# Optimization experiments

Hardware: AMD Instinct MI355X
Metric: run time of the kernel (lower is better)

## Reference

```python
import jax, jax.numpy as jnp
import numpy as np

B, T, P, D, S, R = 4, 128, 256, 512, 64, 8  # batch, window, patches, d_model, n_state, dt_rank


def setup_inputs() -> dict:
    key = jax.random.key(0)
    ks = jax.random.split(key, 8)
    sc = 0.02  # weight init scale
    return {
        "X": jax.random.normal(ks[0], (B, T, P, D), jnp.float32),
        "H0": jnp.zeros((B, P, S), jnp.float32),
        "a_hat": jax.random.normal(ks[1], (S,), jnp.float32),
        "U_w": jax.random.normal(ks[2], (S, D), jnp.float32) * sc,
        "sB_w": jax.random.normal(ks[3], (S, D), jnp.float32) * sc,
        "sB_b": jnp.zeros((S,), jnp.float32),
        "sC_w": jax.random.normal(ks[4], (S, D), jnp.float32) * sc,
        "sC_b": jnp.zeros((S,), jnp.float32),
        "sD1_w": jax.random.normal(ks[5], (R, D), jnp.float32) * sc,
        "sD1_b": jnp.zeros((R,), jnp.float32),
        "sD2_w": jax.random.normal(ks[6], (1, R), jnp.float32) * sc,
        "sD2_b": jnp.zeros((1,), jnp.float32),
        "ro_w": jax.random.normal(ks[7], (D, S), jnp.float32) * sc,
    }


def reference(X, H0, a_hat, U_w, sB_w, sB_b, sC_w, sC_b, sD1_w, sD1_b, sD2_w, sD2_b, ro_w):
    eps = 1e-12
    logA = -jnp.exp(a_hat)                                    # [S]
    # selective (input-dependent) parameters
    u = jnp.einsum('btpd,sd->btps', X, U_w)                   # [B,T,P,S]
    B_t = jnp.einsum('btpd,sd->btps', X, sB_w) + sB_b
    C_t = jnp.einsum('btpd,sd->btps', X, sC_w) + sC_b
    dt_feat = jax.nn.silu(jnp.einsum('btpd,rd->btpr', X, sD1_w) + sD1_b)
    dt = jax.nn.softplus(jnp.einsum('btpr,or->btpo', dt_feat, sD2_w) + sD2_b)  # [B,T,P,1]
    A = jnp.exp(dt * logA)                                    # [B,T,P,S] via broadcast
    b = (1.0 - A) * (B_t * u)
    # prefix-product scan: h_t = A_t*h_{t-1} + b_t  ->  h_t = P_t*(H0 + cumsum(b/P))
    Pc = jnp.cumprod(jnp.maximum(A, eps), axis=1)             # [B,T,P,S]
    invP = 1.0 / jnp.maximum(Pc, eps)
    c = jnp.cumsum(b * invP, axis=1)
    H_seq = Pc * (H0[:, None] + c)                            # [B,T,P,S]
    Y_seq = jnp.einsum('btps,ds->btpd', C_t * H_seq, ro_w)    # [B,T,P,D]
    Y_seq = Y_seq.reshape(X.shape[0], -1, X.shape[-1])        # [B, T*P, D]
    H_T = H_seq[:, -1]                                        # [B,P,S]
    return (H_seq, Y_seq, H_T)
```

## Files before the change

kernel.cpp:

```cpp
#include <hip/hip_runtime.h>
#include <math.h>

namespace {
constexpr int B_N = 4;
constexpr int T_N = 128;
constexpr int P_N = 256;
constexpr int D_N = 512;
constexpr int S_N = 64;
constexpr int NTH = 512;
constexpr int KC  = 64;

constexpr int XS_OFF  = 0;
constexpr int WS_OFF  = 16384;
constexpr int UB_OFF  = 0;
constexpr int BB_OFF  = 32768;
constexpr int CH_OFF  = 49152;
constexpr int ROS_OFF = 0;
constexpr int DT_OFF  = 65536;
constexpr int LA_OFF  = 66048;
constexpr int LDS_BYTES = 66304;
}

typedef short bf16x8 __attribute__((ext_vector_type(8)));
typedef float f32x4  __attribute__((ext_vector_type(4)));

__device__ __forceinline__ unsigned short f2b(float f) {
    unsigned int x = __float_as_uint(f);
    return (unsigned short)((x + 0x7FFFu + ((x >> 16) & 1u)) >> 16);
}
__device__ __forceinline__ float b2f(unsigned short h) {
    return __uint_as_float(((unsigned int)h) << 16);
}
__device__ __forceinline__ int swz(int row, int col) {
    return row * 64 + (col ^ ((row & 7) << 3));
}

__device__ __forceinline__ void stage16(unsigned short* tile, int row, int col0,
                                        const float* __restrict__ src) {
    float4 v0 = *(const float4*)(src);
    float4 v1 = *(const float4*)(src + 4);
    float4 v2 = *(const float4*)(src + 8);
    float4 v3 = *(const float4*)(src + 12);
    bf16x8 h0, h1;
    h0[0] = (short)f2b(v0.x); h0[1] = (short)f2b(v0.y); h0[2] = (short)f2b(v0.z); h0[3] = (short)f2b(v0.w);
    h0[4] = (short)f2b(v1.x); h0[5] = (short)f2b(v1.y); h0[6] = (short)f2b(v1.z); h0[7] = (short)f2b(v1.w);
    h1[0] = (short)f2b(v2.x); h1[1] = (short)f2b(v2.y); h1[2] = (short)f2b(v2.z); h1[3] = (short)f2b(v2.w);
    h1[4] = (short)f2b(v3.x); h1[5] = (short)f2b(v3.y); h1[6] = (short)f2b(v3.z); h1[7] = (short)f2b(v3.w);
    *(bf16x8*)&tile[swz(row, col0)]     = h0;
    *(bf16x8*)&tile[swz(row, col0 + 8)] = h1;
}

__global__ __launch_bounds__(NTH, 4) void mamba_mfma(
    const float* __restrict__ X, const float* __restrict__ H0,
    const float* __restrict__ a_hat,
    const float* __restrict__ U_w, const float* __restrict__ sB_w, const float* __restrict__ sB_b,
    const float* __restrict__ sC_w, const float* __restrict__ sC_b,
    const float* __restrict__ sD1_w, const float* __restrict__ sD1_b,
    const float* __restrict__ sD2_w, const float* __restrict__ sD2_b,
    const float* __restrict__ ro_w,
    float* __restrict__ Hseq, float* __restrict__ Y, float* __restrict__ HT)
{
    __shared__ __align__(16) char smem[LDS_BYTES];
    unsigned short* XS  = (unsigned short*)(smem + XS_OFF);
    unsigned short* WS  = (unsigned short*)(smem + WS_OFF);
    float*          UBUF= (float*)(smem + UB_OFF);
    unsigned short* BBUF= (unsigned short*)(smem + BB_OFF);
    unsigned short* ROS = (unsigned short*)(smem + ROS_OFF);
    unsigned short* CHB = (unsigned short*)(smem + CH_OFF);
    float*          DTB = (float*)(smem + DT_OFF);
    float*          LA  = (float*)(smem + LA_OFF);

    const int tid  = threadIdx.x;
    const int lane = tid & 63;
    const int wid  = tid >> 6;
    const int wm   = wid >> 2;
    const int wn   = wid & 3;
    const int l15  = lane & 15;
    const int lg   = lane >> 4;
    const int b    = blockIdx.x >> 8;
    const int p    = blockIdx.x & 255;

    if (tid < S_N) LA[tid] = -expf(a_hat[tid]);
    if (tid < 256) ((unsigned int*)(WS + 200 * 64))[tid] = 0;

    f32x4 acc[4][3];
    f32x4 accdt[4];
    #pragma unroll
    for (int mf = 0; mf < 4; ++mf) {
        #pragma unroll
        for (int q = 0; q < 4; ++q) accdt[mf][q] = 0.0f;
        #pragma unroll
        for (int nf = 0; nf < 3; ++nf)
            #pragma unroll
            for (int q = 0; q < 4; ++q) acc[mf][nf][q] = 0.0f;
    }

    const int xr = tid >> 2;
    const int xq = tid & 3;
    const float* xbase = X + (((size_t)b * T_N + xr) * P_N + p) * D_N + xq * 16;

    for (int kc0 = 0; kc0 < D_N; kc0 += KC) {
        stage16(XS, xr, xq * 16, xbase + kc0);
        for (int idx = tid; idx < 800; idx += NTH) {
            int row = idx >> 2, kq = idx & 3;
            const float* wsrc;
            if (row < 64)       wsrc = U_w   + (size_t)row * D_N;
            else if (row < 128) wsrc = sB_w  + (size_t)(row - 64) * D_N;
            else if (row < 192) wsrc = sC_w  + (size_t)(row - 128) * D_N;
            else                wsrc = sD1_w + (size_t)(row - 192) * D_N;
            stage16(WS, row, kq * 16, wsrc + kc0 + kq * 16);
        }
        __syncthreads();
        #pragma unroll
        for (int kf = 0; kf < 2; ++kf) {
            const int kb = kf * 32 + lg * 8;
            bf16x8 a[4];
            #pragma unroll
            for (int mf = 0; mf < 4; ++mf)
                a[mf] = *(const bf16x8*)&XS[swz(wm * 64 + mf * 16 + l15, kb)];
            #pragma unroll
            for (int nf = 0; nf < 3; ++nf) {
                bf16x8 bb = *(const bf16x8*)&WS[swz(wn * 48 + nf * 16 + l15, kb)];
                #pragma unroll
                for (int mf = 0; mf < 4; ++mf)
                    acc[mf][nf] = __builtin_amdgcn_mfma_f32_16x16x32_bf16(a[mf], bb, acc[mf][nf], 0, 0, 0);
            }
            if (wn == 0) {
                bf16x8 bd = *(const bf16x8*)&WS[swz(192 + l15, kb)];
                #pragma unroll
                for (int mf = 0; mf < 4; ++mf)
                    accdt[mf] = __builtin_amdgcn_mfma_f32_16x16x32_bf16(a[mf], bd, accdt[mf], 0, 0, 0);
            }
        }
        __syncthreads();
    }

    #pragma unroll
    for (int nf = 0; nf < 3; ++nf) {
        const int abscol = wn * 48 + nf * 16 + l15;
        const int kind = abscol >> 6;
        const int s = abscol & 63;
        const float bias = (kind == 0) ? 0.0f : (kind == 1 ? sB_b[s] : sC_b[s]);
        #pragma unroll
        for (int mf = 0; mf < 4; ++mf) {
            #pragma unroll
            for (int q = 0; q < 4; ++q) {
                const int t = wm * 64 + mf * 16 + lg * 4 + q;
                const float v = acc[mf][nf][q] + bias;
                if (kind == 0)      UBUF[t * 64 + s] = v;
                else if (kind == 1) BBUF[t * 64 + s] = f2b(v);
                else                CHB[swz(t, s)]   = f2b(v);
            }
        }
    }
    if (wn == 0) {
        const float w2 = (l15 < 8) ? sD2_w[l15] : 0.0f;
        const float b1 = (l15 < 8) ? sD1_b[l15] : 0.0f;
        const float b2 = sD2_b[0];
        #pragma unroll
        for (int mf = 0; mf < 4; ++mf) {
            #pragma unroll
            for (int q = 0; q < 4; ++q) {
                float z = accdt[mf][q] + b1;
                float w = (z / (1.0f + expf(-z))) * w2;
                w = (l15 < 8) ? w : 0.0f;
                w += __shfl_xor(w, 1);
                w += __shfl_xor(w, 2);
                w += __shfl_xor(w, 4);
                if (l15 == 0) {
                    float zz = w + b2;
                    DTB[wm * 64 + mf * 16 + lg * 4 + q] = (zz > 20.0f) ? zz : log1pf(expf(zz));
                }
            }
        }
    }
    __syncthreads();

    if (tid < 64) {
        const int s = tid;
        const float la = LA[s];
        const float h0 = H0[((size_t)b * P_N + p) * S_N + s];
        float Pcv = 1.0f, cv = 0.0f, Hv = 0.0f;
        float* hout = Hseq + ((size_t)b * T_N * P_N + p) * S_N + s;
        for (int t = 0; t < T_N; ++t) {
            const float Av = expf(DTB[t] * la);
            const float bv = (1.0f - Av) * (b2f(BBUF[t * 64 + s]) * UBUF[t * 64 + s]);
            Pcv *= fmaxf(Av, 1e-12f);
            cv += bv * (1.0f / fmaxf(Pcv, 1e-12f));
            Hv = Pcv * (h0 + cv);
            hout[(size_t)t * P_N * S_N] = Hv;
            const int e = swz(t, s);
            CHB[e] = f2b(b2f(CHB[e]) * Hv);
        }
        HT[((size_t)b * P_N + p) * S_N + s] = Hv;
    }
    __syncthreads();

    for (int pp = 0; pp < 2; ++pp) {
        #pragma unroll
        for (int i = 0; i < 2; ++i) {
            const int idx = i * 512 + tid;
            const int row = idx >> 2, kq = idx & 3;
            stage16(ROS, row, kq * 16, ro_w + ((size_t)(pp * 256 + row)) * S_N + kq * 16);
        }
        __syncthreads();
        f32x4 yacc[4][4];
        #pragma unroll
        for (int mf = 0; mf < 4; ++mf)
            #pragma unroll
            for (int nf = 0; nf < 4; ++nf)
                #pragma unroll
                for (int q = 0; q < 4; ++q) yacc[mf][nf][q] = 0.0f;
        #pragma unroll
        for (int kf = 0; kf < 2; ++kf) {
            const int kb = kf * 32 + lg * 8;
            bf16x8 a[4];
            #pragma unroll
            for (int mf = 0; mf < 4; ++mf)
                a[mf] = *(const bf16x8*)&CHB[swz(wm * 64 + mf * 16 + l15, kb)];
            #pragma unroll
            for (int nf = 0; nf < 4; ++nf) {
                bf16x8 bb = *(const bf16x8*)&ROS[swz(wn * 64 + nf * 16 + l15, kb)];
                #pragma unroll
                for (int mf = 0; mf < 4; ++mf)
                    yacc[mf][nf] = __builtin_amdgcn_mfma_f32_16x16x32_bf16(a[mf], bb, yacc[mf][nf], 0, 0, 0);
            }
        }
        #pragma unroll
        for (int mf = 0; mf < 4; ++mf) {
            const int t0 = wm * 64 + mf * 16 + lg * 4;
            float* ybase = Y + (((size_t)b * T_N + t0) * P_N + p) * D_N + pp * 256 + wn * 64 + l15;
            #pragma unroll
            for (int nf = 0; nf < 4; ++nf) {
                #pragma unroll
                for (int q = 0; q < 4; ++q)
                    ybase[(size_t)q * P_N * D_N + nf * 16] = yacc[mf][nf][q];
            }
        }
        if (pp == 0) __syncthreads();
    }
}

extern "C" void kernel_launch(void* const* d_in, const int* in_sizes, int n_in,
                              void* d_out, int out_size, void* d_ws, size_t ws_size,
                              hipStream_t stream) {
    const float* X     = (const float*)d_in[0];
    const float* H0    = (const float*)d_in[1];
    const float* a_hat = (const float*)d_in[2];
    const float* U_w   = (const float*)d_in[3];
    const float* sB_w  = (const float*)d_in[4];
    const float* sB_b  = (const float*)d_in[5];
    const float* sC_w  = (const float*)d_in[6];
    const float* sC_b  = (const float*)d_in[7];
    const float* sD1_w = (const float*)d_in[8];
    const float* sD1_b = (const float*)d_in[9];
    const float* sD2_w = (const float*)d_in[10];
    const float* sD2_b = (const float*)d_in[11];
    const float* ro_w  = (const float*)d_in[12];

    float* out   = (float*)d_out;
    float* HseqP = out;
    float* YP    = out + (size_t)B_N * T_N * P_N * S_N;
    float* HTP   = YP  + (size_t)B_N * T_N * P_N * D_N;

    hipLaunchKernelGGL(mamba_mfma, dim3(B_N * P_N), dim3(NTH), 0, stream,
                       X, H0, a_hat, U_w, sB_w, sB_b, sC_w, sC_b,
                       sD1_w, sD1_b, sD2_w, sD2_b, ro_w, HseqP, YP, HTP);
}
```

Baseline: 180.0 us.

## Shrink LDS footprint and register use to raise occupancy, prefetch X tiles

Stores the u projection in bf16 instead of fp32, which packs the post-GEMM buffers tighter and cuts LDS from about 66KB to about 50KB. The readout GEMM is split into four 128-column passes so fewer accumulator registers are live, and launch bounds are raised to target six waves per SIMD. X chunks are prefetched into registers one K-step ahead, and the bf16 conversion uses packed intrinsics. The costs are extra precision loss on u, more barriers in the readout loop, and possible register spilling under the tighter launch bound.

```diff
diff --git a/kernel.cpp b/kernel.cpp
--- a/kernel.cpp
+++ b/kernel.cpp
@@ -1,4 +1,5 @@
 #include <hip/hip_runtime.h>
+#include <hip/hip_bf16.h>
 #include <math.h>
 
 namespace {
@@ -13,12 +14,12 @@
 constexpr int XS_OFF  = 0;
 constexpr int WS_OFF  = 16384;
 constexpr int UB_OFF  = 0;
-constexpr int BB_OFF  = 32768;
-constexpr int CH_OFF  = 49152;
+constexpr int BB_OFF  = 16384;
+constexpr int CH_OFF  = 32768;
 constexpr int ROS_OFF = 0;
-constexpr int DT_OFF  = 65536;
-constexpr int LA_OFF  = 66048;
-constexpr int LDS_BYTES = 66304;
+constexpr int DT_OFF  = 49152;
+constexpr int LA_OFF  = 49664;
+constexpr int LDS_BYTES = 49920;
 }
 
 typedef short bf16x8 __attribute__((ext_vector_type(8)));
@@ -31,26 +32,31 @@
 __device__ __forceinline__ float b2f(unsigned short h) {
     return __uint_as_float(((unsigned int)h) << 16);
 }
+__device__ __forceinline__ unsigned int pk2(float lo, float hi) {
+    union { __hip_bfloat162 h; unsigned int u; } cv;
+    cv.h = __float22bfloat162_rn(float2{lo, hi});
+    return cv.u;
+}
 __device__ __forceinline__ int swz(int row, int col) {
     return row * 64 + (col ^ ((row & 7) << 3));
 }
-
+__device__ __forceinline__ void cvtstore8(unsigned short* dst, float4 a, float4 b) {
+    uint4 r;
+    r.x = pk2(a.x, a.y); r.y = pk2(a.z, a.w);
+    r.z = pk2(b.x, b.y); r.w = pk2(b.z, b.w);
+    *(uint4*)dst = r;
+}
 __device__ __forceinline__ void stage16(unsigned short* tile, int row, int col0,
                                         const float* __restrict__ src) {
     float4 v0 = *(const float4*)(src);
     float4 v1 = *(const float4*)(src + 4);
     float4 v2 = *(const float4*)(src + 8);
     float4 v3 = *(const float4*)(src + 12);
-    bf16x8 h0, h1;
-    h0[0] = (short)f2b(v0.x); h0[1] = (short)f2b(v0.y); h0[2] = (short)f2b(v0.z); h0[3] = (short)f2b(v0.w);
-    h0[4] = (short)f2b(v1.x); h0[5] = (short)f2b(v1.y); h0[6] = (short)f2b(v1.z); h0[7] = (short)f2b(v1.w);
-    h1[0] = (short)f2b(v2.x); h1[1] = (short)f2b(v2.y); h1[2] = (short)f2b(v2.z); h1[3] = (short)f2b(v2.w);
-    h1[4] = (short)f2b(v3.x); h1[5] = (short)f2b(v3.y); h1[6] = (short)f2b(v3.z); h1[7] = (short)f2b(v3.w);
-    *(bf16x8*)&tile[swz(row, col0)]     = h0;
-    *(bf16x8*)&tile[swz(row, col0 + 8)] = h1;
-}
-
-__global__ __launch_bounds__(NTH, 4) void mamba_mfma(
+    cvtstore8(&tile[swz(row, col0)],     v0, v1);
+    cvtstore8(&tile[swz(row, col0 + 8)], v2, v3);
+}
+
+__global__ __launch_bounds__(NTH, 6) void mamba_mfma(
     const float* __restrict__ X, const float* __restrict__ H0,
     const float* __restrict__ a_hat,
     const float* __restrict__ U_w, const float* __restrict__ sB_w, const float* __restrict__ sB_b,
@@ -63,8 +69,8 @@
     __shared__ __align__(16) char smem[LDS_BYTES];
     unsigned short* XS  = (unsigned short*)(smem + XS_OFF);
     unsigned short* WS  = (unsigned short*)(smem + WS_OFF);
-    float*          UBUF= (float*)(smem + UB_OFF);
-    unsigned short* BBUF= (unsigned short*)(smem + BB_OFF);
+    unsigned short* UB  = (unsigned short*)(smem + UB_OFF);
+    unsigned short* BB  = (unsigned short*)(smem + BB_OFF);
     unsigned short* ROS = (unsigned short*)(smem + ROS_OFF);
     unsigned short* CHB = (unsigned short*)(smem + CH_OFF);
     float*          DTB = (float*)(smem + DT_OFF);
@@ -99,8 +105,14 @@
     const int xq = tid & 3;
     const float* xbase = X + (((size_t)b * T_N + xr) * P_N + p) * D_N + xq * 16;
 
-    for (int kc0 = 0; kc0 < D_N; kc0 += KC) {
-        stage16(XS, xr, xq * 16, xbase + kc0);
+    float4 xa = *(const float4*)(xbase);
+    float4 xb = *(const float4*)(xbase + 4);
+    float4 xc = *(const float4*)(xbase + 8);
+    float4 xd = *(const float4*)(xbase + 12);
+
+    for (int kc = 0; kc < D_N / KC; ++kc) {
+        cvtstore8(&XS[swz(xr, xq * 16)],     xa, xb);
+        cvtstore8(&XS[swz(xr, xq * 16 + 8)], xc, xd);
         for (int idx = tid; idx < 800; idx += NTH) {
             int row = idx >> 2, kq = idx & 3;
             const float* wsrc;
@@ -108,9 +120,16 @@
             else if (row < 128) wsrc = sB_w  + (size_t)(row - 64) * D_N;
             else if (row < 192) wsrc = sC_w  + (size_t)(row - 128) * D_N;
             else                wsrc = sD1_w + (size_t)(row - 192) * D_N;
-            stage16(WS, row, kq * 16, wsrc + kc0 + kq * 16);
+            stage16(WS, row, kq * 16, wsrc + kc * KC + kq * 16);
         }
         __syncthreads();
+        if (kc + 1 < D_N / KC) {
+            const float* nx = xbase + (kc + 1) * KC;
+            xa = *(const float4*)(nx);
+            xb = *(const float4*)(nx + 4);
+            xc = *(const float4*)(nx + 8);
+            xd = *(const float4*)(nx + 12);
+        }
         #pragma unroll
         for (int kf = 0; kf < 2; ++kf) {
             const int kb = kf * 32 + lg * 8;
@@ -147,9 +166,9 @@
             for (int q = 0; q < 4; ++q) {
                 const int t = wm * 64 + mf * 16 + lg * 4 + q;
                 const float v = acc[mf][nf][q] + bias;
-                if (kind == 0)      UBUF[t * 64 + s] = v;
-                else if (kind == 1) BBUF[t * 64 + s] = f2b(v);
-                else                CHB[swz(t, s)]   = f2b(v);
+                if (kind == 0)      UB[t * 64 + s] = f2b(v);
+                else if (kind == 1) BB[t * 64 + s] = f2b(v);
+                else                CHB[swz(t, s)] = f2b(v);
             }
         }
     }
@@ -184,7 +203,7 @@
         float* hout = Hseq + ((size_t)b * T_N * P_N + p) * S_N + s;
         for (int t = 0; t < T_N; ++t) {
             const float Av = expf(DTB[t] * la);
-            const float bv = (1.0f - Av) * (b2f(BBUF[t * 64 + s]) * UBUF[t * 64 + s]);
+            const float bv = (1.0f - Av) * (b2f(BB[t * 64 + s]) * b2f(UB[t * 64 + s]));
             Pcv *= fmaxf(Av, 1e-12f);
             cv += bv * (1.0f / fmaxf(Pcv, 1e-12f));
             Hv = Pcv * (h0 + cv);
@@ -196,19 +215,17 @@
     }
     __syncthreads();
 
-    for (int pp = 0; pp < 2; ++pp) {
-        #pragma unroll
-        for (int i = 0; i < 2; ++i) {
-            const int idx = i * 512 + tid;
-            const int row = idx >> 2, kq = idx & 3;
-            stage16(ROS, row, kq * 16, ro_w + ((size_t)(pp * 256 + row)) * S_N + kq * 16);
+    for (int pp = 0; pp < 4; ++pp) {
+        {
+            const int row = tid >> 2, kq = tid & 3;
+            stage16(ROS, row, kq * 16, ro_w + ((size_t)(pp * 128 + row)) * S_N + kq * 16);
         }
         __syncthreads();
-        f32x4 yacc[4][4];
+        f32x4 yacc[4][2];
         #pragma unroll
         for (int mf = 0; mf < 4; ++mf)
             #pragma unroll
-            for (int nf = 0; nf < 4; ++nf)
+            for (int nf = 0; nf < 2; ++nf)
                 #pragma unroll
                 for (int q = 0; q < 4; ++q) yacc[mf][nf][q] = 0.0f;
         #pragma unroll
@@ -219,8 +236,8 @@
             for (int mf = 0; mf < 4; ++mf)
                 a[mf] = *(const bf16x8*)&CHB[swz(wm * 64 + mf * 16 + l15, kb)];
             #pragma unroll
-            for (int nf = 0; nf < 4; ++nf) {
-                bf16x8 bb = *(const bf16x8*)&ROS[swz(wn * 64 + nf * 16 + l15, kb)];
+            for (int nf = 0; nf < 2; ++nf) {
+                bf16x8 bb = *(const bf16x8*)&ROS[swz(wn * 32 + nf * 16 + l15, kb)];
                 #pragma unroll
                 for (int mf = 0; mf < 4; ++mf)
                     yacc[mf][nf] = __builtin_amdgcn_mfma_f32_16x16x32_bf16(a[mf], bb, yacc[mf][nf], 0, 0, 0);
@@ -229,15 +246,15 @@
         #pragma unroll
         for (int mf = 0; mf < 4; ++mf) {
             const int t0 = wm * 64 + mf * 16 + lg * 4;
-            float* ybase = Y + (((size_t)b * T_N + t0) * P_N + p) * D_N + pp * 256 + wn * 64 + l15;
-            #pragma unroll
-            for (int nf = 0; nf < 4; ++nf) {
+            float* ybase = Y + (((size_t)b * T_N + t0) * P_N + p) * D_N + pp * 128 + wn * 32 + l15;
+            #pragma unroll
+            for (int nf = 0; nf < 2; ++nf) {
                 #pragma unroll
                 for (int q = 0; q < 4; ++q)
                     ybase[(size_t)q * P_N * D_N + nf * 16] = yacc[mf][nf][q];
             }
         }
-        if (pp == 0) __syncthreads();
+        if (pp < 3) __syncthreads();
     }
 }
 
```

New measurement: 424.0 us. 2.36x slower.
